# Performance work log

Hardware: AMD Instinct MI355X
Metric: run time of the kernel (lower is better)

Reference implementation:

```python
import jax, jax.numpy as jnp
import numpy as np

N_NODES = 100000
N_EDGES = 1600000
IN_DIM = 128
HID = 128
BATCH = 16384


def gcn_conv(x, W, b, src, dst, norm, n_nodes):
    # PyG GCNConv: h = x @ W; aggregate norm-weighted messages; add bias.
    h = x @ W                      # [N, H]
    msg = h[src] * norm[:, None]   # [E+N, H] gather + scale
    out = jax.ops.segment_sum(msg, dst, num_segments=n_nodes)
    return out + b


def setup_inputs() -> dict:
    key = jax.random.key(0)
    ks = jax.random.split(key, 12)
    x = jax.random.normal(ks[0], (N_NODES, IN_DIM), dtype=jnp.float32)
    edge_index = jax.random.randint(ks[1], (2, N_EDGES), 0, N_NODES, dtype=jnp.int64)
    src_idx = jax.random.randint(ks[2], (BATCH,), 0, N_NODES, dtype=jnp.int64)
    tgt_idx = jax.random.randint(ks[3], (BATCH,), 0, N_NODES, dtype=jnp.int64)
    s = 1.0 / np.sqrt(HID)
    Wc0 = jax.random.uniform(ks[4], (IN_DIM, HID), jnp.float32, -s, s)
    Wc1 = jax.random.uniform(ks[5], (HID, HID), jnp.float32, -s, s)
    Wc2 = jax.random.uniform(ks[6], (HID, HID), jnp.float32, -s, s)
    bc0 = jnp.zeros((HID,), jnp.float32)
    bc1 = jnp.zeros((HID,), jnp.float32)
    bc2 = jnp.zeros((HID,), jnp.float32)
    s2 = 1.0 / np.sqrt(3 * HID)
    Ww = jax.random.uniform(ks[7], (3 * HID, HID), jnp.float32, -s2, s2)
    bw = jax.random.uniform(ks[8], (HID,), jnp.float32, -s2, s2)
    Wp = jax.random.uniform(ks[9], (3 * HID, HID), jnp.float32, -s2, s2)
    bp = jax.random.uniform(ks[10], (HID,), jnp.float32, -s2, s2)
    return {"x": x, "edge_index": edge_index, "src_idx": src_idx, "tgt_idx": tgt_idx,
            "Wc0": Wc0, "bc0": bc0, "Wc1": Wc1, "bc1": bc1, "Wc2": Wc2, "bc2": bc2,
            "Ww": Ww, "bw": bw, "Wp": Wp, "bp": bp}


def reference(x, edge_index, src_idx, tgt_idx, Wc0, bc0, Wc1, bc1, Wc2, bc2, Ww, bw, Wp, bp):
    n = x.shape[0]
    loops = jnp.arange(n, dtype=edge_index.dtype)
    src = jnp.concatenate([edge_index[0], loops])  # GCN adds self-loops
    dst = jnp.concatenate([edge_index[1], loops])
    deg = jax.ops.segment_sum(jnp.ones_like(src, dtype=x.dtype), dst, num_segments=n)
    dinv = jnp.where(deg > 0, jax.lax.rsqrt(deg), 0.0)
    norm = dinv[src] * dinv[dst]   # symmetric normalization D^-1/2 A D^-1/2

    x1 = jax.nn.relu(gcn_conv(x, Wc0, bc0, src, dst, norm, n))   # dropout p=0 -> identity
    x2 = jax.nn.relu(gcn_conv(x1, Wc1, bc1, src, dst, norm, n))
    x3 = jax.nn.relu(gcn_conv(x2, Wc2, bc2, src, dst, norm, n))
    xcat = jnp.concatenate([x1, x2, x3], axis=1)   # [N, 3H]
    xW = xcat @ Ww + bw   # [N, H]
    xp = xcat @ Wp + bp   # [N, H]
    # bilinear score: bmm of [B,1,H] x [B,H,1] == rowwise dot product
    sv = jnp.sum(xp[src_idx] * xW[tgt_idx], axis=-1)   # [B]
    return sv
```

## Files before the change

### kernel.cpp

```cpp
#include <hip/hip_runtime.h>
#include <hip/hip_bf16.h>

#define N_NODES 100000
#define N_EDGES 1600000
#define BATCH   16384
#define HID     128

#define SHIFT 9
#define BSZ   512
#define NB    196
#define EPB   8192

typedef __attribute__((ext_vector_type(8))) short bf16x8;
typedef __attribute__((ext_vector_type(4))) float fx4;
typedef __attribute__((ext_vector_type(2))) float fx2;

__device__ inline short f2bf(float f) {
    unsigned u = __builtin_bit_cast(unsigned, f);
    unsigned r = (u + 0x7FFF + ((u >> 16) & 1)) >> 16;
    return (short)r;
}
__device__ inline float bf2f(short s) {
    unsigned u = ((unsigned)(unsigned short)s) << 16;
    return __builtin_bit_cast(float, u);
}


__global__ __launch_bounds__(256) void k_bhist(const int* __restrict__ dst,
                                               int* __restrict__ bcnt, int E) {
    __shared__ int lh[NB];
    int t = threadIdx.x;
    for (int j = t; j < NB; j += 256) lh[j] = 0;
    __syncthreads();
    int base = blockIdx.x * 4096;
    int n = min(4096, E - base);
    for (int i = t; i < n; i += 256) atomicAdd(&lh[dst[base + i] >> SHIFT], 1);
    __syncthreads();
    for (int j = t; j < NB; j += 256)
        if (lh[j]) atomicAdd(&bcnt[j], lh[j]);
}

__global__ void k_bscan(const int* __restrict__ bcnt, int* __restrict__ bbase,
                        int* __restrict__ bcur, int* __restrict__ offsets) {
    __shared__ int sh[256];
    int t = threadIdx.x;
    int c = (t < NB) ? bcnt[t] : 0;
    sh[t] = c;
    __syncthreads();
    for (int off = 1; off < 256; off <<= 1) {
        int v = 0;
        if (t >= off) v = sh[t - off];
        __syncthreads();
        if (t >= off) sh[t] += v;
        __syncthreads();
    }
    int incl = sh[t];
    int excl = incl - c;
    if (t < NB) { bbase[t] = excl; bcur[t] = excl; }
    if (t == NB - 1) { bbase[NB] = incl; offsets[N_NODES] = incl; }
}

__global__ __launch_bounds__(256) void k_passA(
    const int* __restrict__ edge, int* __restrict__ bcur,
    unsigned* __restrict__ tmp, int E) {
    __shared__ unsigned staged[EPB];
    __shared__ unsigned char bkt[EPB];
    __shared__ int lh[NB], lstart[NB], gbase[NB], lcur[NB];
    int t = threadIdx.x;
    int base = blockIdx.x * EPB;
    int n = min(EPB, E - base);
    for (int j = t; j < NB; j += 256) lh[j] = 0;
    __syncthreads();
    for (int i = t; i < n; i += 256)
        atomicAdd(&lh[edge[E + base + i] >> SHIFT], 1);
    __syncthreads();
    if (t == 0) {
        int run = 0;
        for (int b = 0; b < NB; ++b) { lstart[b] = run; run += lh[b]; }
    }
    __syncthreads();
    if (t < NB) {
        gbase[t] = atomicAdd(&bcur[t], lh[t]);
        lcur[t] = lstart[t];
    }
    __syncthreads();
    for (int i = t; i < n; i += 256) {
        int s = edge[base + i];
        int d = edge[E + base + i];
        int b = d >> SHIFT;
        unsigned p = (unsigned)s | ((unsigned)(d & (BSZ - 1)) << 17);
        int pos = atomicAdd(&lcur[b], 1);
        staged[pos] = p;
        bkt[pos] = (unsigned char)b;
    }
    __syncthreads();
    for (int i = t; i < n; i += 256) {
        int b = bkt[i];
        tmp[gbase[b] + (i - lstart[b])] = staged[i];
    }
}

__global__ __launch_bounds__(256) void k_passB(
    const unsigned* __restrict__ tmp, const int* __restrict__ bbase,
    int* __restrict__ offsets, float* __restrict__ dinv,
    int* __restrict__ col) {
    __shared__ int lh[BSZ];
    __shared__ int lsum[256];
    int b = blockIdx.x, t = threadIdx.x;
    int begin = bbase[b], end = bbase[b + 1];
    lh[t] = 0; lh[t + 256] = 0;
    __syncthreads();
    for (int i = begin + t; i < end; i += 256)
        atomicAdd(&lh[tmp[i] >> 17], 1);
    __syncthreads();
    int c0 = lh[2 * t], c1 = lh[2 * t + 1];
    int tsum = c0 + c1;
    lsum[t] = tsum;
    __syncthreads();
    for (int off = 1; off < 256; off <<= 1) {
        int v = 0;
        if (t >= off) v = lsum[t - off];
        __syncthreads();
        if (t >= off) lsum[t] += v;
        __syncthreads();
    }
    int texcl = lsum[t] - tsum;
    int node0 = (b << SHIFT) + 2 * t;
    if (node0 < N_NODES) {
        offsets[node0] = begin + texcl;
        dinv[node0] = rsqrtf((float)c0 + 1.f);
    }
    if (node0 + 1 < N_NODES) {
        offsets[node0 + 1] = begin + texcl + c0;
        dinv[node0 + 1] = rsqrtf((float)c1 + 1.f);
    }
    __syncthreads();
    lh[2 * t] = texcl;
    lh[2 * t + 1] = texcl + c0;
    __syncthreads();
    for (int i = begin + t; i < end; i += 1024) {
        int i1 = i + 256, i2 = i + 512, i3 = i + 768;
        unsigned p0 = tmp[i];
        unsigned p1 = (i1 < end) ? tmp[i1] : 0u;
        unsigned p2 = (i2 < end) ? tmp[i2] : 0u;
        unsigned p3 = (i3 < end) ? tmp[i3] : 0u;
        int pos0 = begin + atomicAdd(&lh[p0 >> 17], 1);
        col[pos0] = (int)(p0 & 0x1FFFFu);
        if (i1 < end) { int q = begin + atomicAdd(&lh[p1 >> 17], 1); col[q] = (int)(p1 & 0x1FFFFu); }
        if (i2 < end) { int q = begin + atomicAdd(&lh[p2 >> 17], 1); col[q] = (int)(p2 & 0x1FFFFu); }
        if (i3 < end) { int q = begin + atomicAdd(&lh[p3 >> 17], 1); col[q] = (int)(p3 & 0x1FFFFu); }
    }
}


__global__ void k_prepW(const float* __restrict__ Wc0, const float* __restrict__ Wc1,
                        const float* __restrict__ Wc2, const float* __restrict__ Wp,
                        const float* __restrict__ Ww, short* __restrict__ wI) {
    int c = blockIdx.x;
    const float* src;
    int koff = 0;
    if (c == 0) src = Wc0;
    else if (c == 1) src = Wc1;
    else if (c == 2) src = Wc2;
    else if (c < 6) { src = Wp; koff = (c - 3) * 128; }
    else { src = Ww; koff = (c - 6) * 128; }
    short* d = wI + (size_t)c * 32768;
    for (int i = threadIdx.x; i < 16384; i += 256) {
        int k = i >> 7, n = i & 127;
        float v = src[(size_t)(koff + k) * 128 + n];
        short h = f2bf(v);
        short l = f2bf(v - bf2f(h));
        int c16 = k >> 3, j = k & 7;
        d[n * 256 + c16 * 16 + j] = h;
        d[n * 256 + c16 * 16 + 8 + j] = l;
    }
}


__device__ inline void stage_tile(char* __restrict__ buf, const char* __restrict__ A,
                                  int tile, int maxRow, int t) {
    int rowBase = tile << 6;
#pragma unroll
    for (int j = 0; j < 8; ++j) {
        int s = (j << 8) + t;
        int row = s >> 5;
        int cpos = s & 31;
        int c = cpos ^ (row & 7);
        int gr = rowBase + row;
        if (gr > maxRow) gr = maxRow;
        const char* src = A + ((size_t)gr << 9) + (c << 4);
        char* dst = buf + (((j << 8) + (t & 192)) << 4);
        __builtin_amdgcn_global_load_lds(
            (const __attribute__((address_space(1))) unsigned*)src,
            (__attribute__((address_space(3))) unsigned*)dst, 16, 0, 0);
    }
}

template<int ISF32>
__global__ __launch_bounds__(256) void k_sgemm(
    const char* __restrict__ A, const short* __restrict__ WI,
    short* __restrict__ outb, const float* __restrict__ scale, int M) {
    __shared__ __align__(16) char lds[65536];
    int t = threadIdx.x;
    int lane = t & 63, wave = t >> 6;
    int wm = wave >> 1, wn = wave & 1;
    int l15 = lane & 15, g = lane >> 4;
    int colBase = wn << 6;
    int rq = g << 2;

    bf16x8 Bh[4][4], Bl[4][4];
#pragma unroll
    for (int ks = 0; ks < 4; ++ks)
#pragma unroll
        for (int fc = 0; fc < 4; ++fc) {
            int c = colBase + (fc << 4) + l15;
            const short* bp = &WI[((size_t)c << 8) + (((ks << 2) + g) << 4)];
            Bh[ks][fc] = *(const bf16x8*)bp;
            Bl[ks][fc] = *(const bf16x8*)(bp + 8);
        }

    int nT = (M + 63) >> 6;
    int maxRow = M - 1;
    int tile = blockIdx.x;
    if (tile < nT) stage_tile(lds, A, tile, maxRow, t);
    int cur = 0;

    for (; tile < nT; tile += gridDim.x) {
        __syncthreads();
        int nxt = tile + gridDim.x;
        if (nxt < nT) stage_tile(lds + ((cur ^ 1) << 15), A, nxt, maxRow, t);
        char* buf = lds + (cur << 15);

        fx4 acc[2][4];
#pragma unroll
        for (int i = 0; i < 2; ++i)
#pragma unroll
            for (int j = 0; j < 4; ++j) {
                acc[i][j][0] = 0.f; acc[i][j][1] = 0.f;
                acc[i][j][2] = 0.f; acc[i][j][3] = 0.f;
            }

#pragma unroll
        for (int ks = 0; ks < 4; ++ks) {
            bf16x8 ah[2], al[2];
#pragma unroll
            for (int fr = 0; fr < 2; ++fr) {
                int row = (wm << 5) + (fr << 4) + l15;
                int c0 = (ks << 3) + (g << 1);
                const char* p0 = buf + (row << 9) + ((c0 ^ (row & 7)) << 4);
                const char* p1 = buf + (row << 9) + (((c0 + 1) ^ (row & 7)) << 4);
                if (ISF32) {
                    float v[8];
                    *(float4*)&v[0] = *(const float4*)p0;
                    *(float4*)&v[4] = *(const float4*)p1;
#pragma unroll
                    for (int j = 0; j < 8; ++j) {
                        short hb = f2bf(v[j]);
                        ah[fr][j] = hb;
                        al[fr][j] = f2bf(v[j] - bf2f(hb));
                    }
                } else {
                    ah[fr] = *(const bf16x8*)p0;
                    al[fr] = *(const bf16x8*)p1;
                }
            }
#pragma unroll
            for (int fc = 0; fc < 4; ++fc) {
                acc[0][fc] = __builtin_amdgcn_mfma_f32_16x16x32_bf16(ah[0], Bh[ks][fc], acc[0][fc], 0, 0, 0);
                acc[0][fc] = __builtin_amdgcn_mfma_f32_16x16x32_bf16(ah[0], Bl[ks][fc], acc[0][fc], 0, 0, 0);
                acc[0][fc] = __builtin_amdgcn_mfma_f32_16x16x32_bf16(al[0], Bh[ks][fc], acc[0][fc], 0, 0, 0);
                acc[1][fc] = __builtin_amdgcn_mfma_f32_16x16x32_bf16(ah[1], Bh[ks][fc], acc[1][fc], 0, 0, 0);
                acc[1][fc] = __builtin_amdgcn_mfma_f32_16x16x32_bf16(ah[1], Bl[ks][fc], acc[1][fc], 0, 0, 0);
                acc[1][fc] = __builtin_amdgcn_mfma_f32_16x16x32_bf16(al[1], Bh[ks][fc], acc[1][fc], 0, 0, 0);
            }
        }

        __builtin_amdgcn_s_barrier();

        short* scr = (short*)buf + wave * 2304;
        int rowBaseG = tile << 6;
#pragma unroll
        for (int fr = 0; fr < 2; ++fr)
#pragma unroll
            for (int rg = 0; rg < 4; ++rg) {
                int rl = (fr << 4) + rq + rg;
                int R = rowBaseG + (wm << 5) + rl;
                float sc = (R < M) ? scale[R] : 0.f;
#pragma unroll
                for (int fc = 0; fc < 4; ++fc)
                    scr[rl * 72 + (fc << 4) + l15] = f2bf(acc[fr][fc][rg] * sc);
            }
        int rr = lane >> 1, half = lane & 1;
        int R = rowBaseG + (wm << 5) + rr;
        if (R < M) {
            const short* sp = &scr[rr * 72 + (half << 5)];
            short* dp = &outb[((size_t)R << 7) + colBase + (half << 5)];
            ((uint4*)dp)[0] = *(const uint4*)(sp);
            ((uint4*)dp)[1] = *(const uint4*)(sp + 8);
            ((uint4*)dp)[2] = *(const uint4*)(sp + 16);
            ((uint4*)dp)[3] = *(const uint4*)(sp + 24);
        }
        cur ^= 1;
    }
}


__device__ inline void addrow(uint4 u, fx2* a) {
    a[0] += (fx2){__builtin_bit_cast(float, u.x << 16),
                  __builtin_bit_cast(float, u.x & 0xFFFF0000u)};
    a[1] += (fx2){__builtin_bit_cast(float, u.y << 16),
                  __builtin_bit_cast(float, u.y & 0xFFFF0000u)};
    a[2] += (fx2){__builtin_bit_cast(float, u.z << 16),
                  __builtin_bit_cast(float, u.z & 0xFFFF0000u)};
    a[3] += (fx2){__builtin_bit_cast(float, u.w << 16),
                  __builtin_bit_cast(float, u.w & 0xFFFF0000u)};
}

__device__ inline void agg_body(const short* __restrict__ h,
                                const int* __restrict__ col,
                                const int* __restrict__ offs,
                                const float* __restrict__ dinv,
                                const float* __restrict__ bias,
                                short* __restrict__ xoI,
                                int v, int orow) {
    int lane = threadIdx.x & 63;
    int g = lane >> 4;
    int li = lane & 15;
    int beg = offs[v], end = offs[v + 1];
    float dv = dinv[v];
    fx2 a4[4] = {{0.f,0.f},{0.f,0.f},{0.f,0.f},{0.f,0.f}};
    if (g == 0)
        addrow(*(const uint4*)&h[(size_t)v * 128 + (li << 3)], a4);
    int e = beg + g;
    for (; e + 12 < end; e += 16) {
        int s0 = col[e], s1 = col[e + 4], s2 = col[e + 8], s3 = col[e + 12];
        uint4 u0 = *(const uint4*)&h[(size_t)s0 * 128 + (li << 3)];
        uint4 u1 = *(const uint4*)&h[(size_t)s1 * 128 + (li << 3)];
        uint4 u2 = *(const uint4*)&h[(size_t)s2 * 128 + (li << 3)];
        uint4 u3 = *(const uint4*)&h[(size_t)s3 * 128 + (li << 3)];
        addrow(u0, a4); addrow(u1, a4); addrow(u2, a4); addrow(u3, a4);
    }
    for (; e < end; e += 4)
        addrow(*(const uint4*)&h[(size_t)col[e] * 128 + (li << 3)], a4);

    float a[8];
#pragma unroll
    for (int j = 0; j < 4; ++j) { a[2 * j] = a4[j][0]; a[2 * j + 1] = a4[j][1]; }
#pragma unroll
    for (int off = 16; off <= 32; off <<= 1)
#pragma unroll
        for (int j = 0; j < 8; ++j) a[j] += __shfl_xor(a[j], off);
    if (g == 0) {
        bf16x8 hh, ll;
#pragma unroll
        for (int j = 0; j < 8; ++j) {
            float o = fmaxf(fmaf(a[j], dv, bias[(li << 3) + j]), 0.f);
            short hb = f2bf(o);
            hh[j] = hb;
            ll[j] = f2bf(o - bf2f(hb));
        }
        short* dst = &xoI[((size_t)orow << 8) + (li << 4)];
        *(bf16x8*)dst = hh;
        *(bf16x8*)(dst + 8) = ll;
    }
}

__global__ __launch_bounds__(256) void k_agg(
    const short* __restrict__ h, const int* __restrict__ col,
    const int* __restrict__ offs, const float* __restrict__ dinv,
    const float* __restrict__ bias, short* __restrict__ xoI, int n) {
    int v = (blockIdx.x << 2) + (threadIdx.x >> 6);
    if (v >= n) return;
    agg_body(h, col, offs, dinv, bias, xoI, v, v);
}

__global__ __launch_bounds__(256) void k_agg3(
    const short* __restrict__ h, const int* __restrict__ col,
    const int* __restrict__ offs, const float* __restrict__ dinv,
    const float* __restrict__ bias, short* __restrict__ xoI,
    const int* __restrict__ sidx, const int* __restrict__ tidx) {
    int i = (blockIdx.x << 2) + (threadIdx.x >> 6);
    if (i >= 2 * BATCH) return;
    int v = (i < BATCH) ? sidx[i] : tidx[i - BATCH];
    agg_body(h, col, offs, dinv, bias, xoI, v, i);
}


__global__ __launch_bounds__(256) void k_pq(
    const short* __restrict__ a1I, const short* __restrict__ a2I,
    const short* __restrict__ x3I, const short* __restrict__ wI,
    const int* __restrict__ sidx, const int* __restrict__ tidx,
    const float* __restrict__ bp, const float* __restrict__ bw,
    float* __restrict__ out) {
    __shared__ float Ps[32][132];
    __shared__ float Qs[32][132];
    int t = threadIdx.x;
    int lane = t & 63, wave = t >> 6;
    int isQ = wave >> 1, wn = wave & 1;
    int l15 = lane & 15;
    int g16 = (lane >> 4) << 4;
    int pairBase = blockIdx.x << 5;
    int colBase = wn << 6;
    const int* gidx = isQ ? tidx : sidx;
    const float* bias = isQ ? bw : bp;
    int r0i = pairBase + l15;
    int r1i = r0i + 16;
    long long n0 = (long long)gidx[r0i];
    long long n1 = (long long)gidx[r1i];

    fx4 acc[2][4];
#pragma unroll
    for (int i = 0; i < 2; ++i)
#pragma unroll
        for (int j = 0; j < 4; ++j) {
            acc[i][j][0] = 0.f; acc[i][j][1] = 0.f;
            acc[i][j][2] = 0.f; acc[i][j][3] = 0.f;
        }

#pragma unroll
    for (int c = 0; c < 3; ++c) {
        const short* AI = (c == 0) ? a1I : (c == 1) ? a2I : x3I;
        long long b0 = (c == 2) ? (long long)(r0i + (isQ << 14)) : n0;
        long long b1 = (c == 2) ? (long long)(r1i + (isQ << 14)) : n1;
        const short* WB = wI + (size_t)(3 + isQ * 3 + c) * 32768;
#pragma unroll
        for (int ks = 0; ks < 4; ++ks) {
            int co = (ks << 6) + g16;
            const short* ap0 = &AI[(b0 << 8) + co];
            const short* ap1 = &AI[(b1 << 8) + co];
            bf16x8 a0h = *(const bf16x8*)ap0;
            bf16x8 a0l = *(const bf16x8*)(ap0 + 8);
            bf16x8 a1h = *(const bf16x8*)ap1;
            bf16x8 a1l = *(const bf16x8*)(ap1 + 8);
#pragma unroll
            for (int fc = 0; fc < 4; ++fc) {
                int cc = colBase + (fc << 4) + l15;
                const short* bpp = &WB[((size_t)cc << 8) + co];
                bf16x8 bh = *(const bf16x8*)bpp;
                bf16x8 bl = *(const bf16x8*)(bpp + 8);
                acc[0][fc] = __builtin_amdgcn_mfma_f32_16x16x32_bf16(a0h, bh, acc[0][fc], 0, 0, 0);
                acc[0][fc] = __builtin_amdgcn_mfma_f32_16x16x32_bf16(a0h, bl, acc[0][fc], 0, 0, 0);
                acc[0][fc] = __builtin_amdgcn_mfma_f32_16x16x32_bf16(a0l, bh, acc[0][fc], 0, 0, 0);
                acc[1][fc] = __builtin_amdgcn_mfma_f32_16x16x32_bf16(a1h, bh, acc[1][fc], 0, 0, 0);
                acc[1][fc] = __builtin_amdgcn_mfma_f32_16x16x32_bf16(a1h, bl, acc[1][fc], 0, 0, 0);
                acc[1][fc] = __builtin_amdgcn_mfma_f32_16x16x32_bf16(a1l, bh, acc[1][fc], 0, 0, 0);
            }
        }
    }

    int rq = (lane >> 4) << 2;
    float (*dst)[132] = isQ ? Qs : Ps;
#pragma unroll
    for (int fr = 0; fr < 2; ++fr) {
#pragma unroll
        for (int fc = 0; fc < 4; ++fc) {
            int cg = colBase + (fc << 4) + l15;
            float bv = bias[cg];
#pragma unroll
            for (int rg = 0; rg < 4; ++rg)
                dst[(fr << 4) + rq + rg][cg] = acc[fr][fc][rg] + bv;
        }
    }
    __syncthreads();

    int p = t >> 3, seg = t & 7;
    const float* pr = &Ps[p][seg * 16];
    const float* qr = &Qs[p][seg * 16];
    float s = 0.f;
#pragma unroll
    for (int j = 0; j < 16; ++j) s += pr[j] * qr[j];
    s += __shfl_xor(s, 1);
    s += __shfl_xor(s, 2);
    s += __shfl_xor(s, 4);
    if (seg == 0) out[pairBase + p] = s;
}


extern "C" void kernel_launch(void* const* d_in, const int* in_sizes, int n_in,
                              void* d_out, int out_size, void* d_ws, size_t ws_size,
                              hipStream_t stream) {
    const float* x    = (const float*)d_in[0];
    const int*   edge = (const int*)d_in[1];
    const int*   sidx = (const int*)d_in[2];
    const int*   tidx = (const int*)d_in[3];
    const float* Wc0  = (const float*)d_in[4];
    const float* bc0  = (const float*)d_in[5];
    const float* Wc1  = (const float*)d_in[6];
    const float* bc1  = (const float*)d_in[7];
    const float* Wc2  = (const float*)d_in[8];
    const float* bc2  = (const float*)d_in[9];
    const float* Ww   = (const float*)d_in[10];
    const float* bw   = (const float*)d_in[11];
    const float* Wp   = (const float*)d_in[12];
    const float* bp   = (const float*)d_in[13];
    float* out = (float*)d_out;

    char* base = (char*)d_ws;
    size_t off = 0;
    auto alloc = [&](size_t bytes) -> char* {
        char* p = base + off;
        off = (off + bytes + 255) & ~(size_t)255;
        return p;
    };
    const size_t ISZ = (size_t)N_NODES * 256 * sizeof(short);
    const size_t XSZ = (size_t)2 * BATCH * 256 * sizeof(short);
    short* a1I  = (short*)alloc(ISZ);
    short* a2I  = (short*)alloc(ISZ);
    short* x3I  = (short*)alloc(XSZ);
    short* hbf  = (short*)alloc((size_t)N_NODES * HID * sizeof(short));
    int*   offsets = (int*)alloc((size_t)(N_NODES + 1) * sizeof(int));
    int*   colArr  = (int*)alloc((size_t)N_EDGES * sizeof(int));
    unsigned* tmp  = (unsigned*)alloc((size_t)N_EDGES * sizeof(unsigned));
    float* dinv    = (float*)alloc((size_t)N_NODES * sizeof(float));
    int*   bcnt    = (int*)alloc(256 * sizeof(int));
    int*   bbase   = (int*)alloc(256 * sizeof(int));
    int*   bcur    = (int*)alloc(256 * sizeof(int));
    short* wI      = (short*)alloc((size_t)9 * 32768 * sizeof(short));
    (void)ws_size; (void)in_sizes; (void)n_in; (void)out_size;

    hipMemsetAsync(bcnt, 0, NB * sizeof(int), stream);
    k_bhist<<<(N_EDGES + 4095) / 4096, 256, 0, stream>>>(edge + N_EDGES, bcnt, N_EDGES);
    k_bscan<<<1, 256, 0, stream>>>(bcnt, bbase, bcur, offsets);
    k_passA<<<(N_EDGES + EPB - 1) / EPB, 256, 0, stream>>>(edge, bcur, tmp, N_EDGES);
    k_passB<<<NB, 256, 0, stream>>>(tmp, bbase, offsets, dinv, colArr);

    k_prepW<<<9, 256, 0, stream>>>(Wc0, Wc1, Wc2, Wp, Ww, wI);

    const int aggGrid  = (N_NODES + 3) / 4;
    const int agg3Grid = (2 * BATCH) / 4;
#define WI(c) (wI + (size_t)(c) * 32768)

    k_sgemm<1><<<512, 256, 0, stream>>>((const char*)x, WI(0), hbf, dinv, N_NODES);
    k_agg<<<aggGrid, 256, 0, stream>>>(hbf, colArr, offsets, dinv, bc0, a1I, N_NODES);

    k_sgemm<0><<<512, 256, 0, stream>>>((const char*)a1I, WI(1), hbf, dinv, N_NODES);
    k_agg<<<aggGrid, 256, 0, stream>>>(hbf, colArr, offsets, dinv, bc1, a2I, N_NODES);

    k_sgemm<0><<<512, 256, 0, stream>>>((const char*)a2I, WI(2), hbf, dinv, N_NODES);
    k_agg3<<<agg3Grid, 256, 0, stream>>>(hbf, colArr, offsets, dinv, bc2, x3I, sidx, tidx);

    k_pq<<<BATCH / 32, 256, 0, stream>>>(a1I, a2I, x3I, wI, sidx, tidx, bp, bw, out);
}
```

Before: 379.5 us.

## Shrink GEMM row tile to 32 and split columns across four waves

```diff
diff --git a/kernel.cpp b/kernel.cpp
--- a/kernel.cpp
+++ b/kernel.cpp
@@ -179,9 +179,9 @@
 
 __device__ inline void stage_tile(char* __restrict__ buf, const char* __restrict__ A,
                                   int tile, int maxRow, int t) {
-    int rowBase = tile << 6;
-#pragma unroll
-    for (int j = 0; j < 8; ++j) {
+    int rowBase = tile << 5;
+#pragma unroll
+    for (int j = 0; j < 4; ++j) {
         int s = (j << 8) + t;
         int row = s >> 5;
         int cpos = s & 31;
@@ -200,26 +200,25 @@
 __global__ __launch_bounds__(256) void k_sgemm(
     const char* __restrict__ A, const short* __restrict__ WI,
     short* __restrict__ outb, const float* __restrict__ scale, int M) {
-    __shared__ __align__(16) char lds[65536];
+    __shared__ __align__(16) char lds[32768];
     int t = threadIdx.x;
     int lane = t & 63, wave = t >> 6;
-    int wm = wave >> 1, wn = wave & 1;
     int l15 = lane & 15, g = lane >> 4;
-    int colBase = wn << 6;
+    int colBase = wave << 5;
     int rq = g << 2;
 
-    bf16x8 Bh[4][4], Bl[4][4];
+    bf16x8 Bh[4][2], Bl[4][2];
 #pragma unroll
     for (int ks = 0; ks < 4; ++ks)
 #pragma unroll
-        for (int fc = 0; fc < 4; ++fc) {
+        for (int fc = 0; fc < 2; ++fc) {
             int c = colBase + (fc << 4) + l15;
             const short* bp = &WI[((size_t)c << 8) + (((ks << 2) + g) << 4)];
             Bh[ks][fc] = *(const bf16x8*)bp;
             Bl[ks][fc] = *(const bf16x8*)(bp + 8);
         }
 
-    int nT = (M + 63) >> 6;
+    int nT = (M + 31) >> 5;
     int maxRow = M - 1;
     int tile = blockIdx.x;
     if (tile < nT) stage_tile(lds, A, tile, maxRow, t);
@@ -228,14 +227,14 @@
     for (; tile < nT; tile += gridDim.x) {
         __syncthreads();
         int nxt = tile + gridDim.x;
-        if (nxt < nT) stage_tile(lds + ((cur ^ 1) << 15), A, nxt, maxRow, t);
-        char* buf = lds + (cur << 15);
-
-        fx4 acc[2][4];
+        if (nxt < nT) stage_tile(lds + ((cur ^ 1) << 14), A, nxt, maxRow, t);
+        char* buf = lds + (cur << 14);
+
+        fx4 acc[2][2];
 #pragma unroll
         for (int i = 0; i < 2; ++i)
 #pragma unroll
-            for (int j = 0; j < 4; ++j) {
+            for (int j = 0; j < 2; ++j) {
                 acc[i][j][0] = 0.f; acc[i][j][1] = 0.f;
                 acc[i][j][2] = 0.f; acc[i][j][3] = 0.f;
             }
@@ -245,7 +244,7 @@
             bf16x8 ah[2], al[2];
 #pragma unroll
             for (int fr = 0; fr < 2; ++fr) {
-                int row = (wm << 5) + (fr << 4) + l15;
+                int row = (fr << 4) + l15;
                 int c0 = (ks << 3) + (g << 1);
                 const char* p0 = buf + (row << 9) + ((c0 ^ (row & 7)) << 4);
                 const char* p1 = buf + (row << 9) + (((c0 + 1) ^ (row & 7)) << 4);
@@ -265,7 +264,7 @@
                 }
             }
 #pragma unroll
-            for (int fc = 0; fc < 4; ++fc) {
+            for (int fc = 0; fc < 2; ++fc) {
                 acc[0][fc] = __builtin_amdgcn_mfma_f32_16x16x32_bf16(ah[0], Bh[ks][fc], acc[0][fc], 0, 0, 0);
                 acc[0][fc] = __builtin_amdgcn_mfma_f32_16x16x32_bf16(ah[0], Bl[ks][fc], acc[0][fc], 0, 0, 0);
                 acc[0][fc] = __builtin_amdgcn_mfma_f32_16x16x32_bf16(al[0], Bh[ks][fc], acc[0][fc], 0, 0, 0);
@@ -277,28 +276,26 @@
 
         __builtin_amdgcn_s_barrier();
 
-        short* scr = (short*)buf + wave * 2304;
-        int rowBaseG = tile << 6;
+        short* relay = (short*)buf + wave * 1280;
+        int rowBaseG = tile << 5;
 #pragma unroll
         for (int fr = 0; fr < 2; ++fr)
 #pragma unroll
             for (int rg = 0; rg < 4; ++rg) {
                 int rl = (fr << 4) + rq + rg;
-                int R = rowBaseG + (wm << 5) + rl;
+                int R = rowBaseG + rl;
                 float sc = (R < M) ? scale[R] : 0.f;
 #pragma unroll
-                for (int fc = 0; fc < 4; ++fc)
-                    scr[rl * 72 + (fc << 4) + l15] = f2bf(acc[fr][fc][rg] * sc);
+                for (int fc = 0; fc < 2; ++fc)
+                    relay[rl * 40 + (fc << 4) + l15] = f2bf(acc[fr][fc][rg] * sc);
             }
-        int rr = lane >> 1, half = lane & 1;
-        int R = rowBaseG + (wm << 5) + rr;
+        int rr = lane >> 1, seg = lane & 1;
+        int R = rowBaseG + rr;
         if (R < M) {
-            const short* sp = &scr[rr * 72 + (half << 5)];
-            short* dp = &outb[((size_t)R << 7) + colBase + (half << 5)];
-            ((uint4*)dp)[0] = *(const uint4*)(sp);
-            ((uint4*)dp)[1] = *(const uint4*)(sp + 8);
-            ((uint4*)dp)[2] = *(const uint4*)(sp + 16);
-            ((uint4*)dp)[3] = *(const uint4*)(sp + 24);
+            const short* sp = &relay[rr * 40 + (seg << 4)];
+            short* dp = &outb[((size_t)R << 7) + colBase + (seg << 4)];
+            ((uint4*)dp)[0] = ((const uint4*)sp)[0];
+            ((uint4*)dp)[1] = ((const uint4*)sp)[1];
         }
         cur ^= 1;
     }
@@ -528,15 +525,16 @@
 
     const int aggGrid  = (N_NODES + 3) / 4;
     const int agg3Grid = (2 * BATCH) / 4;
+    const int gemmGrid = 768;
 #define WI(c) (wI + (size_t)(c) * 32768)
 
-    k_sgemm<1><<<512, 256, 0, stream>>>((const char*)x, WI(0), hbf, dinv, N_NODES);
+    k_sgemm<1><<<gemmGrid, 256, 0, stream>>>((const char*)x, WI(0), hbf, dinv, N_NODES);
     k_agg<<<aggGrid, 256, 0, stream>>>(hbf, colArr, offsets, dinv, bc0, a1I, N_NODES);
 
-    k_sgemm<0><<<512, 256, 0, stream>>>((const char*)a1I, WI(1), hbf, dinv, N_NODES);
+    k_sgemm<0><<<gemmGrid, 256, 0, stream>>>((const char*)a1I, WI(1), hbf, dinv, N_NODES);
     k_agg<<<aggGrid, 256, 0, stream>>>(hbf, colArr, offsets, dinv, bc1, a2I, N_NODES);
 
-    k_sgemm<0><<<512, 256, 0, stream>>>((const char*)a2I, WI(2), hbf, dinv, N_NODES);
+    k_sgemm<0><<<gemmGrid, 256, 0, stream>>>((const char*)a2I, WI(2), hbf, dinv, N_NODES);
     k_agg3<<<agg3Grid, 256, 0, stream>>>(hbf, colArr, offsets, dinv, bc2, x3I, sidx, tidx);
 
     k_pq<<<BATCH / 32, 256, 0, stream>>>(a1I, a2I, x3I, wI, sidx, tidx, bp, bw, out);
```

Result: faster. 368.8 us (-2.8%).
